# Performance work log

Measured on AMD Instinct MI355X. Metric: run time of the kernel, lower is better.

Reference implementation:

```python
import jax, jax.numpy as jnp
import numpy as np

C = 256; G = 16; GC = C // G; K = 3; P = K * K
N = 4; H = 64; W = 64
PAD = 1; OFFSET_SCALE = 1.0; LN_EPS = 1e-5


def setup_inputs() -> dict:
    key = jax.random.key(0)
    ks = jax.random.split(key, 8)
    s = 0.02
    return {
        "x": jax.random.normal(ks[0], (N, C, H, W), jnp.float32),
        "dw_w": jax.random.normal(ks[1], (C, 1, K, K), jnp.float32) * s,
        "dw_b": jnp.zeros((C,), jnp.float32),
        "ln_g": jnp.ones((C,), jnp.float32),
        "ln_b": jnp.zeros((C,), jnp.float32),
        "off_w": jax.random.normal(ks[2], (C, G * P * 2), jnp.float32) * s,
        "off_b": jnp.zeros((G * P * 2,), jnp.float32),
        "mask_w": jax.random.normal(ks[3], (C, G * P), jnp.float32) * s,
        "mask_b": jnp.zeros((G * P,), jnp.float32),
        "inp_w": jax.random.normal(ks[4], (C, C), jnp.float32) * s,
        "inp_b": jnp.zeros((C,), jnp.float32),
        "out_w": jax.random.normal(ks[5], (C, C), jnp.float32) * s,
        "out_b": jnp.zeros((C,), jnp.float32),
    }


def _dcnv3_nchw(x, dw_w, dw_b, ln_g, ln_b, off_w, off_b, mask_w, mask_b,
                inp_w, inp_b, out_w, out_b):
    # NCHW -> NHWC (wrapper permute)
    xn = jnp.transpose(x, (0, 2, 3, 1))                      # (N,H,W,C)
    x_proj = xn @ inp_w + inp_b                              # input_proj

    # offset/mask branch: depthwise conv (NCHW) -> LayerNorm (channels-last) -> GELU
    x1 = jax.lax.conv_general_dilated(
        x, dw_w, window_strides=(1, 1), padding=((PAD, PAD), (PAD, PAD)),
        dimension_numbers=("NCHW", "OIHW", "NCHW"), feature_group_count=C)
    x1 = jnp.transpose(x1, (0, 2, 3, 1)) + dw_b
    mu = x1.mean(-1, keepdims=True)
    var = ((x1 - mu) ** 2).mean(-1, keepdims=True)
    x1 = (x1 - mu) * jax.lax.rsqrt(var + LN_EPS) * ln_g + ln_b
    x1 = jax.nn.gelu(x1, approximate=False)

    offset = (x1 @ off_w + off_b).reshape(N, H, W, G, P, 2)  # (x,y) pairs
    mask = jax.nn.softmax((x1 @ mask_w + mask_b).reshape(N, H, W, G, P), axis=-1)

    # pad sampled feature map with zeros (F.pad before sampling)
    xp = jnp.pad(x_proj, ((0, 0), (PAD, PAD), (PAD, PAD), (0, 0)))
    Hin, Win = H + 2 * PAD, W + 2 * PAD
    xg = xp.reshape(N, Hin, Win, G, GC)

    # reference points, normalized by padded size
    ref_y = (jnp.arange(H, dtype=jnp.float32) + PAD + 0.5) / Hin
    ref_x = (jnp.arange(W, dtype=jnp.float32) + PAD + 0.5) / Win
    ref = jnp.stack([jnp.broadcast_to(ref_x[None, :], (H, W)),
                     jnp.broadcast_to(ref_y[:, None], (H, W))], -1)  # (H,W,2)

    # dilation grid: x varies in the outer loop (torch meshgrid 'ij')
    d = jnp.arange(K, dtype=jnp.float32) - (K - 1) // 2     # [-1,0,1]
    gx = jnp.repeat(d, K) / Win
    gy = jnp.tile(d, K) / Hin
    grid = jnp.stack([gx, gy], -1)                           # (P,2)

    norm = jnp.array([Win, Hin], jnp.float32)
    loc = (ref[None, :, :, None, None, :] + grid * OFFSET_SCALE
           + offset * OFFSET_SCALE / norm)                   # (N,H,W,G,P,2)

    # grid_sample bilinear, align_corners=False, zero padding
    px = loc[..., 0] * Win - 0.5
    py = loc[..., 1] * Hin - 0.5
    x0 = jnp.floor(px); y0 = jnp.floor(py)
    wx = px - x0; wy = py - y0
    x0i = x0.astype(jnp.int32); y0i = y0.astype(jnp.int32)

    n_idx = jnp.arange(N)[:, None, None, None, None]
    g_idx = jnp.arange(G)[None, None, None, :, None]

    def corner(iy, ix, w):
        valid = (iy >= 0) & (iy < Hin) & (ix >= 0) & (ix < Win)
        v = xg[n_idx, jnp.clip(iy, 0, Hin - 1), jnp.clip(ix, 0, Win - 1), g_idx]
        wgt = jnp.where(valid, w, 0.0) * mask                # fold mask into weights
        return jnp.einsum("nhwgp,nhwgpc->nhwgc", wgt, v)

    out = (corner(y0i, x0i, (1 - wy) * (1 - wx))
           + corner(y0i, x0i + 1, (1 - wy) * wx)
           + corner(y0i + 1, x0i, wy * (1 - wx))
           + corner(y0i + 1, x0i + 1, wy * wx))               # (N,H,W,G,GC)

    out = out.reshape(N, H, W, C) @ out_w + out_b            # output_proj
    return jnp.transpose(out, (0, 3, 1, 2))                  # NHWC -> NCHW


def reference(x, dw_w, dw_b, ln_g, ln_b, off_w, off_b, mask_w, mask_b,
              inp_w, inp_b, out_w, out_b):
    return _dcnv3_nchw(x, dw_w, dw_b, ln_g, ln_b, off_w, off_b,
                       mask_w, mask_b, inp_w, inp_b, out_w, out_b)
```

## Files before the change

### kernel.cpp

```cpp
#include <hip/hip_runtime.h>
#include <hip/hip_bf16.h>
#include <math.h>


using bf16x8 = __attribute__((ext_vector_type(8))) short;
using f32x4  = __attribute__((ext_vector_type(4))) float;

#define GLOBAL_AS __attribute__((address_space(1)))
#define LDS_AS    __attribute__((address_space(3)))

static __device__ inline void g2lds16(const void* g, void* l) {
  __builtin_amdgcn_global_load_lds((const GLOBAL_AS int*)g, (LDS_AS int*)l, 16, 0, 0);
}
static __device__ inline unsigned short f2bf(float v) {
  __hip_bfloat16 b = __float2bfloat16(v);
  return *reinterpret_cast<unsigned short*>(&b);
}
static __device__ inline float us2f(unsigned short u) {
  union { unsigned u; float f; } c; c.u = ((unsigned)u) << 16; return c.f;
}

__global__ __launch_bounds__(256) void prep_k(
    const float* __restrict__ inp_w, const float* __restrict__ off_w,
    const float* __restrict__ off_b, const float* __restrict__ mask_w,
    const float* __restrict__ mask_b, const float* __restrict__ out_w,
    __hip_bfloat16* __restrict__ BtI, __hip_bfloat16* __restrict__ BtOM,
    __hip_bfloat16* __restrict__ BtO, float* __restrict__ bOM)
{
  int b = blockIdx.x, t = threadIdx.x;
  if (b < 256) {
    int n = b;
    BtI[n * 256 + t] = __float2bfloat16(inp_w[t * 256 + n]);
  } else if (b < 768) {
    int n = b - 256;
    float v = 0.f;
    if (n < 288) v = off_w[t * 288 + n];
    else if (n < 432) v = mask_w[t * 144 + (n - 288)];
    BtOM[n * 256 + t] = __float2bfloat16(v);
    if (b == 256) {
      for (int idx = t; idx < 512; idx += 256) {
        float bv = (idx < 288) ? off_b[idx] : ((idx < 432) ? mask_b[idx - 288] : 0.f);
        bOM[idx] = bv;
      }
    }
  } else {
    int n = b - 768;
    BtO[n * 256 + t] = __float2bfloat16(out_w[t * 256 + n]);
  }
}

__global__ __launch_bounds__(256) void gemm_i(
    const float* __restrict__ x, const __hip_bfloat16* __restrict__ BtI,
    const float* __restrict__ inp_b, __hip_bfloat16* __restrict__ xpu)
{
  __shared__ __align__(16) char smem[12288];
  float* Asf = (float*)smem;
  short* Bs  = (short*)(smem + 8192);
  const int t = threadIdx.x;
  const int n0 = blockIdx.x * 64;
  const size_t m0 = (size_t)blockIdx.y * 64;
  const int n4 = (int)(m0 >> 12), hw0 = (int)(m0 & 4095);

  const int wave = t >> 6, lane = t & 63;
  const int quad = lane >> 4, lr = lane & 15;
  const int wm = wave >> 1, wn = wave & 1;

  f32x4 acc[2][2];
  #pragma unroll
  for (int i = 0; i < 2; ++i)
    #pragma unroll
    for (int j = 0; j < 2; ++j)
      acc[i][j] = (f32x4){0.f, 0.f, 0.f, 0.f};

  for (int kt = 0; kt < 256; kt += 32) {
    #pragma unroll
    for (int j = 0; j < 2; ++j) {
      int idx = j * 256 + t;
      int kk = idx >> 4, px4 = (idx & 15) * 4;
      g2lds16(x + (size_t)n4 * 1048576 + (size_t)(kt + kk) * 4096 + hw0 + px4,
              (char*)Asf + idx * 16);
    }
    g2lds16(BtI + (size_t)(n0 + (t >> 2)) * 256 + kt + (t & 3) * 8,
            (char*)Bs + t * 16);
    __syncthreads();
    bf16x8 bfv[2];
    #pragma unroll
    for (int ni = 0; ni < 2; ++ni)
      bfv[ni] = *(const bf16x8*)&Bs[(wn * 32 + ni * 16 + lr) * 32 + quad * 8];
    #pragma unroll
    for (int mi = 0; mi < 2; ++mi) {
      int m = wm * 32 + mi * 16 + lr;
      bf16x8 af;
      #pragma unroll
      for (int j2 = 0; j2 < 8; ++j2)
        ((unsigned short*)&af)[j2] = f2bf(Asf[(quad * 8 + j2) * 64 + m]);
      #pragma unroll
      for (int ni = 0; ni < 2; ++ni)
        acc[mi][ni] = __builtin_amdgcn_mfma_f32_16x16x32_bf16(af, bfv[ni], acc[mi][ni], 0, 0, 0);
    }
    __syncthreads();
  }

  #pragma unroll
  for (int mi = 0; mi < 2; ++mi) {
    #pragma unroll
    for (int ni = 0; ni < 2; ++ni) {
      int col = n0 + wn * 32 + ni * 16 + lr;
      float bv = inp_b[col];
      #pragma unroll
      for (int reg = 0; reg < 4; ++reg) {
        size_t m = m0 + wm * 32 + mi * 16 + quad * 4 + reg;
        xpu[m * 256 + col] = __float2bfloat16(acc[mi][ni][reg] + bv);
      }
    }
  }
}

__global__ __launch_bounds__(1024) void stage2_k(
    const float* __restrict__ x,
    const float* __restrict__ dw_w, const float* __restrict__ dw_b,
    const float* __restrict__ ln_g, const float* __restrict__ ln_b,
    const __hip_bfloat16* __restrict__ BtOM, const float* __restrict__ bOM,
    __hip_bfloat16* __restrict__ om)
{
  __shared__ __align__(16) char smem[62464];
  unsigned short* x1t = (unsigned short*)smem;
  unsigned short* xs  = (unsigned short*)(smem + 33792);
  float* wgt  = (float*)(smem + 33792 + 13824);
  float* psq  = (float*)(smem + 33792 + 13824 + 1152);
  float* murs = (float*)(smem + 33792 + 13824 + 1152 + 8192);
  short* Bs   = (short*)(smem + 33792);

  const int blk = blockIdx.x;
  const int n4 = blk >> 6, h = blk & 63;
  const int t = threadIdx.x;
  const int w = t & 63, q = t >> 6;

  float s1 = 0.f, s2 = 0.f;
  for (int chunk = 0; chunk < 8; ++chunk) {
    const int ch0 = chunk * 32;
    if (t < 768) {
      int seg = t >> 3, part = t & 7;
      int r = seg >> 5, c = seg & 31;
      int px0 = part * 8;
      int hh = h + r - 1;
      float4 v0 = {0,0,0,0}, v1 = {0,0,0,0};
      if ((unsigned)hh < 64u) {
        const float* src = x + (size_t)n4 * 1048576 + (size_t)(ch0 + c) * 4096 + hh * 64 + px0;
        v0 = *(const float4*)src;
        v1 = *(const float4*)(src + 4);
      }
      uint4 u;
      u.x = (unsigned)f2bf(v0.x) | ((unsigned)f2bf(v0.y) << 16);
      u.y = (unsigned)f2bf(v0.z) | ((unsigned)f2bf(v0.w) << 16);
      u.z = (unsigned)f2bf(v1.x) | ((unsigned)f2bf(v1.y) << 16);
      u.w = (unsigned)f2bf(v1.z) | ((unsigned)f2bf(v1.w) << 16);
      *(uint4*)&xs[(r * 32 + c) * 72 + px0] = u;
    }
    if (t < 288) {
      int p = t >> 5, lc = t & 31;
      wgt[p * 32 + lc] = dw_w[(ch0 + lc) * 9 + p];
    }
    __syncthreads();
    {
      int lc = 2 * q;
      int c = ch0 + lc;
      float a0 = dw_b[c], a1 = dw_b[c + 1];
      #pragma unroll
      for (int p = 0; p < 9; ++p) {
        int dh = p / 3, dwd = p % 3 - 1;
        int ww = w + dwd;
        if ((unsigned)ww < 64u) {
          float wa = wgt[p * 32 + lc], wb = wgt[p * 32 + lc + 1];
          a0 = fmaf(us2f(xs[(dh * 32 + lc) * 72 + ww]), wa, a0);
          a1 = fmaf(us2f(xs[(dh * 32 + lc + 1) * 72 + ww]), wb, a1);
        }
      }
      s1 += a0 + a1;
      s2 = fmaf(a0, a0, fmaf(a1, a1, s2));
      *(unsigned*)&x1t[w * 264 + c] = (unsigned)f2bf(a0) | ((unsigned)f2bf(a1) << 16);
    }
    __syncthreads();
  }

  psq[q * 64 + w] = s1;
  psq[1024 + q * 64 + w] = s2;
  __syncthreads();
  if (t < 64) {
    float a = 0.f, b = 0.f;
    #pragma unroll
    for (int j = 0; j < 16; ++j) { a += psq[j * 64 + t]; b += psq[1024 + j * 64 + t]; }
    float mu = a * (1.f / 256.f);
    murs[t] = mu;
    murs[64 + t] = rsqrtf(b * (1.f / 256.f) - mu * mu + 1e-5f);
  }
  __syncthreads();
  {
    float mu = murs[w], rs = murs[64 + w];
    #pragma unroll
    for (int chunk = 0; chunk < 8; ++chunk) {
      int c = chunk * 32 + 2 * q;
      unsigned pk = *(const unsigned*)&x1t[w * 264 + c];
      float v0 = us2f((unsigned short)(pk & 0xffff));
      float v1 = us2f((unsigned short)(pk >> 16));
      float y0 = fmaf((v0 - mu) * rs, ln_g[c], ln_b[c]);
      float y1 = fmaf((v1 - mu) * rs, ln_g[c + 1], ln_b[c + 1]);
      float g0 = 0.5f * y0 * (1.f + erff(y0 * 0.70710678f));
      float g1 = 0.5f * y1 * (1.f + erff(y1 * 0.70710678f));
      *(unsigned*)&x1t[w * 264 + c] = (unsigned)f2bf(g0) | ((unsigned)f2bf(g1) << 16);
    }
  }

  const int wave = t >> 6, lane = t & 63;
  const int quad = lane >> 4, lr = lane & 15;
  const int wm = wave >> 2, wn = wave & 3;
  f32x4 acc[7];
  #pragma unroll
  for (int i = 0; i < 7; ++i) acc[i] = (f32x4){0.f, 0.f, 0.f, 0.f};

  for (int kt = 0; kt < 256; kt += 32) {
    __syncthreads();
    {
      int col = t >> 2, kq = t & 3;
      g2lds16(BtOM + (size_t)col * 256 + kt + kq * 8, (char*)Bs + t * 16);
      int j = t + 1024;
      if (j < 1792) {
        col = j >> 2; kq = j & 3;
        g2lds16(BtOM + (size_t)col * 256 + kt + kq * 8, (char*)Bs + j * 16);
      }
    }
    __syncthreads();
    bf16x8 af = *(const bf16x8*)&x1t[(wm * 16 + lr) * 264 + kt + quad * 8];
    #pragma unroll
    for (int ni = 0; ni < 7; ++ni) {
      bf16x8 bf = *(const bf16x8*)&Bs[(wn * 112 + ni * 16 + lr) * 32 + quad * 8];
      acc[ni] = __builtin_amdgcn_mfma_f32_16x16x32_bf16(af, bf, acc[ni], 0, 0, 0);
    }
  }

  const size_t pix0 = (size_t)n4 * 4096 + (size_t)h * 64;
  #pragma unroll
  for (int ni = 0; ni < 7; ++ni) {
    int col = wn * 112 + ni * 16 + lr;
    if (col < 432) {
      float bv = bOM[col];
      #pragma unroll
      for (int reg = 0; reg < 4; ++reg) {
        int m = wm * 16 + quad * 4 + reg;
        om[(pix0 + m) * 448 + col] = __float2bfloat16(acc[ni][reg] + bv);
      }
    }
  }
}

__global__ __launch_bounds__(256) void samp_o(
    const __hip_bfloat16* __restrict__ xpu, const __hip_bfloat16* __restrict__ om,
    const __hip_bfloat16* __restrict__ BtO, const float* __restrict__ out_b,
    float* __restrict__ out)
{
  __shared__ __align__(16) char smem[39168];
  unsigned short* oms   = (unsigned short*)smem;
  unsigned short* sampS = (unsigned short*)(smem + 14336);
  short* Bs = (short*)(smem + 22784);
  float* tb = (float*)smem;

  const int bid = blockIdx.x;
  const int region = bid & 7;
  const int qb = bid >> 3;
  const int pix0 = region * 2048 + qb * 16;
  const int n4 = pix0 >> 12, hw0 = pix0 & 4095;
  const int t = threadIdx.x;

  {
    const uint4* gsrc = (const uint4*)(om + (size_t)pix0 * 448);
    uint4* ldst = (uint4*)oms;
    #pragma unroll
    for (int r = 0; r < 4; ++r) {
      int i = t + r * 256;
      if (i < 896) ldst[i] = gsrc[i];
    }
  }
  __syncthreads();

  {
    const int g = t & 15;
    const int pl = t >> 4;
    const int hw = hw0 + pl;
    const int h = hw >> 6, w = hw & 63;

    float mk[9];
    const unsigned short* mp = &oms[pl * 448 + 288 + g * 9];
    float mx = -1e30f;
    #pragma unroll
    for (int p = 0; p < 9; ++p) { mk[p] = us2f(mp[p]); mx = fmaxf(mx, mk[p]); }
    float se = 0.f;
    #pragma unroll
    for (int p = 0; p < 9; ++p) { mk[p] = __expf(mk[p] - mx); se += mk[p]; }
    float inv = 1.f / se;
    #pragma unroll
    for (int p = 0; p < 9; ++p) mk[p] *= inv;

    const unsigned short* op = &oms[pl * 448 + g * 18];
    const __hip_bfloat16* xpg = xpu + (g << 4);
    float ax[16];
    #pragma unroll
    for (int i = 0; i < 16; ++i) ax[i] = 0.f;

    auto corner = [&](int iy, int ix, float wt) {
      if ((unsigned)(iy - 1) >= 64u || (unsigned)(ix - 1) >= 64u) return;
      const __hip_bfloat16* src =
          xpg + ((size_t)((n4 << 12) + (iy - 1) * 64 + (ix - 1)) << 8);
      uint4 u0 = *(const uint4*)src;
      uint4 u1 = *(const uint4*)(src + 8);
      const unsigned uu[8] = {u0.x, u0.y, u0.z, u0.w, u1.x, u1.y, u1.z, u1.w};
      #pragma unroll
      for (int i = 0; i < 8; ++i) {
        float lo = us2f((unsigned short)(uu[i] & 0xffff));
        float hi = us2f((unsigned short)(uu[i] >> 16));
        ax[2 * i + 0] = fmaf(wt, lo, ax[2 * i + 0]);
        ax[2 * i + 1] = fmaf(wt, hi, ax[2 * i + 1]);
      }
    };

    #pragma unroll
    for (int p = 0; p < 9; ++p) {
      float ox = us2f(op[2 * p]), oy = us2f(op[2 * p + 1]);
      float px = (float)(w + p / 3) + ox;
      float py = (float)(h + p % 3) + oy;
      float xf = floorf(px), yf = floorf(py);
      float wx = px - xf, wy = py - yf;
      int ix = (int)xf, iy = (int)yf;
      float m = mk[p];
      corner(iy,     ix,     (1.f - wy) * (1.f - wx) * m);
      corner(iy,     ix + 1, (1.f - wy) * wx * m);
      corner(iy + 1, ix,     wy * (1.f - wx) * m);
      corner(iy + 1, ix + 1, wy * wx * m);
    }

    unsigned short ub[16];
    #pragma unroll
    for (int i = 0; i < 16; ++i) ub[i] = f2bf(ax[i]);
    uint4 u0, u1;
    u0.x = (unsigned)ub[0] | ((unsigned)ub[1] << 16);
    u0.y = (unsigned)ub[2] | ((unsigned)ub[3] << 16);
    u0.z = (unsigned)ub[4] | ((unsigned)ub[5] << 16);
    u0.w = (unsigned)ub[6] | ((unsigned)ub[7] << 16);
    u1.x = (unsigned)ub[8] | ((unsigned)ub[9] << 16);
    u1.y = (unsigned)ub[10] | ((unsigned)ub[11] << 16);
    u1.z = (unsigned)ub[12] | ((unsigned)ub[13] << 16);
    u1.w = (unsigned)ub[14] | ((unsigned)ub[15] << 16);
    *(uint4*)&sampS[pl * 264 + g * 16] = u0;
    *(uint4*)&sampS[pl * 264 + g * 16 + 8] = u1;
  }
  __syncthreads();

  const int wave = t >> 6, lane = t & 63;
  const int quad = lane >> 4, lr = lane & 15;
  f32x4 acc[4];
  #pragma unroll
  for (int i = 0; i < 4; ++i) acc[i] = (f32x4){0.f, 0.f, 0.f, 0.f};

  for (int kt = 0; kt < 256; kt += 32) {
    if (kt) __syncthreads();
    #pragma unroll
    for (int j = 0; j < 4; ++j) {
      int idx = j * 256 + t;
      int col = idx >> 2, kq = idx & 3;
      g2lds16(BtO + (size_t)col * 256 + kt + kq * 8, (char*)Bs + idx * 16);
    }
    __syncthreads();
    bf16x8 af = *(const bf16x8*)&sampS[lr * 264 + kt + quad * 8];
    #pragma unroll
    for (int ni = 0; ni < 4; ++ni) {
      bf16x8 bf = *(const bf16x8*)&Bs[(wave * 64 + ni * 16 + lr) * 32 + quad * 8];
      acc[ni] = __builtin_amdgcn_mfma_f32_16x16x32_bf16(af, bf, acc[ni], 0, 0, 0);
    }
  }
  __syncthreads();

  #pragma unroll
  for (int ni = 0; ni < 4; ++ni) {
    int col = wave * 64 + ni * 16 + lr;
    float bv = out_b[col];
    #pragma unroll
    for (int reg = 0; reg < 4; ++reg)
      tb[col * 17 + quad * 4 + reg] = acc[ni][reg] + bv;
  }
  __syncthreads();

  {
    int co = t;
    float* dst = out + (size_t)(n4 * 256 + co) * 4096 + hw0;
    #pragma unroll
    for (int j = 0; j < 4; ++j) {
      float4 v;
      v.x = tb[co * 17 + j * 4 + 0];
      v.y = tb[co * 17 + j * 4 + 1];
      v.z = tb[co * 17 + j * 4 + 2];
      v.w = tb[co * 17 + j * 4 + 3];
      *(float4*)(dst + j * 4) = v;
    }
  }
}

extern "C" void kernel_launch(void* const* d_in, const int* in_sizes, int n_in,
                              void* d_out, int out_size, void* d_ws, size_t ws_size,
                              hipStream_t stream) {
  const float* x      = (const float*)d_in[0];
  const float* dw_w   = (const float*)d_in[1];
  const float* dw_b   = (const float*)d_in[2];
  const float* ln_g   = (const float*)d_in[3];
  const float* ln_b   = (const float*)d_in[4];
  const float* off_w  = (const float*)d_in[5];
  const float* off_b  = (const float*)d_in[6];
  const float* mask_w = (const float*)d_in[7];
  const float* mask_b = (const float*)d_in[8];
  const float* inp_w  = (const float*)d_in[9];
  const float* inp_b  = (const float*)d_in[10];
  const float* out_w  = (const float*)d_in[11];
  const float* out_b  = (const float*)d_in[12];
  float* out = (float*)d_out;

  char* w0 = (char*)d_ws;
  __hip_bfloat16* xpu  = (__hip_bfloat16*)(w0);
  __hip_bfloat16* om   = (__hip_bfloat16*)(w0 + 8388608);
  __hip_bfloat16* BtI  = (__hip_bfloat16*)(w0 + 23068672);
  __hip_bfloat16* BtOM = (__hip_bfloat16*)(w0 + 23199744);
  __hip_bfloat16* BtO  = (__hip_bfloat16*)(w0 + 23461888);
  float*          bOM  = (float*)(w0 + 23592960);
  if (ws_size < 23595008) return;

  prep_k<<<1024, 256, 0, stream>>>(inp_w, off_w, off_b, mask_w, mask_b, out_w,
                                   BtI, BtOM, BtO, bOM);
  gemm_i<<<dim3(4, 256), 256, 0, stream>>>(x, BtI, inp_b, xpu);
  stage2_k<<<256, 1024, 0, stream>>>(x, dw_w, dw_b, ln_g, ln_b, BtOM, bOM, om);
  samp_o<<<1024, 256, 0, stream>>>(xpu, om, BtO, out_b, out);
}
```

Before: 170.4 us.

## Fuse input projection GEMM into depthwise-conv stage kernel reusing staged x tile

Removes the separate gemm_i kernel and computes the input projection inside stage2_k. It reuses the bf16 copy of the center input row already staged in LDS for the depthwise conv, streaming 32-channel chunks of the inp_w weights alongside. This saves one kernel launch and a second full read of x from global memory. In exchange stage2_k does more work per block, uses more LDS, and keeps more live accumulator registers, which may lower occupancy. The LDS regions are also re-aliased, which needs careful sync ordering.

```diff
diff --git a/kernel.cpp b/kernel.cpp
--- a/kernel.cpp
+++ b/kernel.cpp
@@ -49,92 +49,35 @@
   }
 }
 
-__global__ __launch_bounds__(256) void gemm_i(
-    const float* __restrict__ x, const __hip_bfloat16* __restrict__ BtI,
-    const float* __restrict__ inp_b, __hip_bfloat16* __restrict__ xpu)
-{
-  __shared__ __align__(16) char smem[12288];
-  float* Asf = (float*)smem;
-  short* Bs  = (short*)(smem + 8192);
-  const int t = threadIdx.x;
-  const int n0 = blockIdx.x * 64;
-  const size_t m0 = (size_t)blockIdx.y * 64;
-  const int n4 = (int)(m0 >> 12), hw0 = (int)(m0 & 4095);
-
-  const int wave = t >> 6, lane = t & 63;
-  const int quad = lane >> 4, lr = lane & 15;
-  const int wm = wave >> 1, wn = wave & 1;
-
-  f32x4 acc[2][2];
-  #pragma unroll
-  for (int i = 0; i < 2; ++i)
-    #pragma unroll
-    for (int j = 0; j < 2; ++j)
-      acc[i][j] = (f32x4){0.f, 0.f, 0.f, 0.f};
-
-  for (int kt = 0; kt < 256; kt += 32) {
-    #pragma unroll
-    for (int j = 0; j < 2; ++j) {
-      int idx = j * 256 + t;
-      int kk = idx >> 4, px4 = (idx & 15) * 4;
-      g2lds16(x + (size_t)n4 * 1048576 + (size_t)(kt + kk) * 4096 + hw0 + px4,
-              (char*)Asf + idx * 16);
-    }
-    g2lds16(BtI + (size_t)(n0 + (t >> 2)) * 256 + kt + (t & 3) * 8,
-            (char*)Bs + t * 16);
-    __syncthreads();
-    bf16x8 bfv[2];
-    #pragma unroll
-    for (int ni = 0; ni < 2; ++ni)
-      bfv[ni] = *(const bf16x8*)&Bs[(wn * 32 + ni * 16 + lr) * 32 + quad * 8];
-    #pragma unroll
-    for (int mi = 0; mi < 2; ++mi) {
-      int m = wm * 32 + mi * 16 + lr;
-      bf16x8 af;
-      #pragma unroll
-      for (int j2 = 0; j2 < 8; ++j2)
-        ((unsigned short*)&af)[j2] = f2bf(Asf[(quad * 8 + j2) * 64 + m]);
-      #pragma unroll
-      for (int ni = 0; ni < 2; ++ni)
-        acc[mi][ni] = __builtin_amdgcn_mfma_f32_16x16x32_bf16(af, bfv[ni], acc[mi][ni], 0, 0, 0);
-    }
-    __syncthreads();
-  }
-
-  #pragma unroll
-  for (int mi = 0; mi < 2; ++mi) {
-    #pragma unroll
-    for (int ni = 0; ni < 2; ++ni) {
-      int col = n0 + wn * 32 + ni * 16 + lr;
-      float bv = inp_b[col];
-      #pragma unroll
-      for (int reg = 0; reg < 4; ++reg) {
-        size_t m = m0 + wm * 32 + mi * 16 + quad * 4 + reg;
-        xpu[m * 256 + col] = __float2bfloat16(acc[mi][ni][reg] + bv);
-      }
-    }
-  }
-}
-
 __global__ __launch_bounds__(1024) void stage2_k(
     const float* __restrict__ x,
     const float* __restrict__ dw_w, const float* __restrict__ dw_b,
     const float* __restrict__ ln_g, const float* __restrict__ ln_b,
+    const __hip_bfloat16* __restrict__ BtI, const float* __restrict__ inp_b,
     const __hip_bfloat16* __restrict__ BtOM, const float* __restrict__ bOM,
-    __hip_bfloat16* __restrict__ om)
+    __hip_bfloat16* __restrict__ xpu, __hip_bfloat16* __restrict__ om)
 {
-  __shared__ __align__(16) char smem[62464];
+  __shared__ __align__(16) char smem[65152];
   unsigned short* x1t = (unsigned short*)smem;
   unsigned short* xs  = (unsigned short*)(smem + 33792);
-  float* wgt  = (float*)(smem + 33792 + 13824);
-  float* psq  = (float*)(smem + 33792 + 13824 + 1152);
-  float* murs = (float*)(smem + 33792 + 13824 + 1152 + 8192);
-  short* Bs   = (short*)(smem + 33792);
+  short* BsI  = (short*)(smem + 33792 + 13824);
+  float* wgt  = (float*)(smem + 64000);
+  float* psq  = (float*)(smem + 33792);
+  float* murs = (float*)(smem + 64000);
+  short* BsOM = (short*)(smem + 33792);
 
   const int blk = blockIdx.x;
   const int n4 = blk >> 6, h = blk & 63;
   const int t = threadIdx.x;
   const int w = t & 63, q = t >> 6;
+
+  const int wave = t >> 6, lane = t & 63;
+  const int quad = lane >> 4, lr = lane & 15;
+  const int wm = wave >> 2, wn = wave & 3;
+
+  f32x4 acc_i[4];
+  #pragma unroll
+  for (int i = 0; i < 4; ++i) acc_i[i] = (f32x4){0.f, 0.f, 0.f, 0.f};
 
   float s1 = 0.f, s2 = 0.f;
   for (int chunk = 0; chunk < 8; ++chunk) {
@@ -161,6 +104,7 @@
       int p = t >> 5, lc = t & 31;
       wgt[p * 32 + lc] = dw_w[(ch0 + lc) * 9 + p];
     }
+    g2lds16(BtI + (size_t)(t >> 2) * 256 + ch0 + (t & 3) * 8, (char*)BsI + t * 16);
     __syncthreads();
     {
       int lc = 2 * q;
@@ -180,7 +124,30 @@
       s2 = fmaf(a0, a0, fmaf(a1, a1, s2));
       *(unsigned*)&x1t[w * 264 + c] = (unsigned)f2bf(a0) | ((unsigned)f2bf(a1) << 16);
     }
+    {
+      bf16x8 af;
+      #pragma unroll
+      for (int j = 0; j < 8; ++j)
+        ((unsigned short*)&af)[j] = xs[(32 + quad * 8 + j) * 72 + wm * 16 + lr];
+      #pragma unroll
+      for (int ni = 0; ni < 4; ++ni) {
+        bf16x8 bf = *(const bf16x8*)&BsI[(wn * 64 + ni * 16 + lr) * 32 + quad * 8];
+        acc_i[ni] = __builtin_amdgcn_mfma_f32_16x16x32_bf16(af, bf, acc_i[ni], 0, 0, 0);
+      }
+    }
     __syncthreads();
+  }
+
+  const size_t pix0 = (size_t)n4 * 4096 + (size_t)h * 64;
+  #pragma unroll
+  for (int ni = 0; ni < 4; ++ni) {
+    int col = wn * 64 + ni * 16 + lr;
+    float bv = inp_b[col];
+    #pragma unroll
+    for (int reg = 0; reg < 4; ++reg) {
+      int m = wm * 16 + quad * 4 + reg;
+      xpu[(pix0 + m) * 256 + col] = __float2bfloat16(acc_i[ni][reg] + bv);
+    }
   }
 
   psq[q * 64 + w] = s1;
@@ -211,9 +178,6 @@
     }
   }
 
-  const int wave = t >> 6, lane = t & 63;
-  const int quad = lane >> 4, lr = lane & 15;
-  const int wm = wave >> 2, wn = wave & 3;
   f32x4 acc[7];
   #pragma unroll
   for (int i = 0; i < 7; ++i) acc[i] = (f32x4){0.f, 0.f, 0.f, 0.f};
@@ -222,23 +186,22 @@
     __syncthreads();
     {
       int col = t >> 2, kq = t & 3;
-      g2lds16(BtOM + (size_t)col * 256 + kt + kq * 8, (char*)Bs + t * 16);
+      g2lds16(BtOM + (size_t)col * 256 + kt + kq * 8, (char*)BsOM + t * 16);
       int j = t + 1024;
       if (j < 1792) {
         col = j >> 2; kq = j & 3;
-        g2lds16(BtOM + (size_t)col * 256 + kt + kq * 8, (char*)Bs + j * 16);
+        g2lds16(BtOM + (size_t)col * 256 + kt + kq * 8, (char*)BsOM + j * 16);
       }
     }
     __syncthreads();
     bf16x8 af = *(const bf16x8*)&x1t[(wm * 16 + lr) * 264 + kt + quad * 8];
     #pragma unroll
     for (int ni = 0; ni < 7; ++ni) {
-      bf16x8 bf = *(const bf16x8*)&Bs[(wn * 112 + ni * 16 + lr) * 32 + quad * 8];
+      bf16x8 bf = *(const bf16x8*)&BsOM[(wn * 112 + ni * 16 + lr) * 32 + quad * 8];
       acc[ni] = __builtin_amdgcn_mfma_f32_16x16x32_bf16(af, bf, acc[ni], 0, 0, 0);
     }
   }
 
-  const size_t pix0 = (size_t)n4 * 4096 + (size_t)h * 64;
   #pragma unroll
   for (int ni = 0; ni < 7; ++ni) {
     int col = wn * 112 + ni * 16 + lr;
@@ -432,7 +395,7 @@
 
   prep_k<<<1024, 256, 0, stream>>>(inp_w, off_w, off_b, mask_w, mask_b, out_w,
                                    BtI, BtOM, BtO, bOM);
-  gemm_i<<<dim3(4, 256), 256, 0, stream>>>(x, BtI, inp_b, xpu);
-  stage2_k<<<256, 1024, 0, stream>>>(x, dw_w, dw_b, ln_g, ln_b, BtOM, bOM, om);
+  stage2_k<<<256, 1024, 0, stream>>>(x, dw_w, dw_b, ln_g, ln_b, BtI, inp_b,
+                                     BtOM, bOM, xpu, om);
   samp_o<<<1024, 256, 0, stream>>>(xpu, om, BtO, out_b, out);
 }
```

Result: faster. 164.9 us (-3.2%).
